# Kernel tuning notes

Hardware: AMD Instinct MI355X
Metric: run time of the kernel (lower is better)

## Reference

```python
import jax, jax.numpy as jnp
import numpy as np

LEAKY = 0.2     # PyG GATConv leaky_relu negative slope
BN_EPS = 1e-5

N, E, F_IN = 100000, 1600000, 7
ENC, HID, HEADS = 64, 32, 4
HC = HID * HEADS          # 128
DEC_IN, OUT = 64, 4
N_HIDDEN = 2              # nb_hidden_layers - 1


def gat_conv(z, src, dst, W, a_src, a_dst, b, concat):
    # PyG GATConv (shared lin for src/dst), dropout in eval mode = identity.
    n = z.shape[0]
    H, C = a_src.shape
    h = (z @ W).reshape(n, H, C)                      # [N,H,C]
    al_s = jnp.einsum('nhc,hc->nh', h, a_src)         # [N,H]
    al_d = jnp.einsum('nhc,hc->nh', h, a_dst)
    e = jax.nn.leaky_relu(al_s[src] + al_d[dst], LEAKY)   # [E,H]
    m = jax.ops.segment_max(e, dst, num_segments=n)       # scatter-softmax over in-edges
    ex = jnp.exp(e - m[dst])
    denom = jax.ops.segment_sum(ex, dst, num_segments=n)
    alpha = ex / (denom[dst] + 1e-16)                     # [E,H]
    out = jax.ops.segment_sum(h[src] * alpha[:, :, None], dst, num_segments=n)  # [N,H,C]
    out = out.reshape(n, H * C) if concat else out.mean(axis=1)
    return out + b


def batch_norm(z, gamma, beta):
    # track_running_stats=False -> always use batch statistics (biased var)
    mu = z.mean(axis=0)
    var = z.var(axis=0)
    return gamma * (z - mu) * jax.lax.rsqrt(var + BN_EPS) + beta


def setup_inputs() -> dict:
    key = jax.random.key(0)
    ks = jax.random.split(key, 20)
    g = lambda k, shape, fan: jax.random.normal(k, shape, jnp.float32) * (1.0 / np.sqrt(fan))
    inp = {
        'x': jax.random.normal(ks[0], (N, F_IN), jnp.float32),
        'edge_index': jax.random.randint(ks[1], (2, E), 0, N, jnp.int32),
        'enc_W': g(ks[2], (F_IN, ENC), F_IN),
        'enc_b': jnp.zeros((ENC,), jnp.float32),
        'in_W': g(ks[3], (ENC, HC), ENC),
        'in_att_src': g(ks[4], (HEADS, HID), HID),
        'in_att_dst': g(ks[5], (HEADS, HID), HID),
        'in_b': jnp.zeros((HC,), jnp.float32),
        'hid_W': g(ks[6], (N_HIDDEN, HC, HC), HC),
        'hid_att_src': g(ks[7], (N_HIDDEN, HEADS, HID), HID),
        'hid_att_dst': g(ks[8], (N_HIDDEN, HEADS, HID), HID),
        'hid_b': jnp.zeros((N_HIDDEN, HC), jnp.float32),
        'bn_gamma': jnp.ones((1 + N_HIDDEN, HC), jnp.float32),
        'bn_beta': jnp.zeros((1 + N_HIDDEN, HC), jnp.float32),
        'out_W': g(ks[9], (HC, DEC_IN), HC),           # out heads=1, concat=False
        'out_att_src': g(ks[10], (1, DEC_IN), DEC_IN),
        'out_att_dst': g(ks[11], (1, DEC_IN), DEC_IN),
        'out_b': jnp.zeros((DEC_IN,), jnp.float32),
        'dec_W': g(ks[12], (DEC_IN, OUT), DEC_IN),
        'dec_b': jnp.zeros((OUT,), jnp.float32),
    }
    return inp


def reference(x, edge_index, enc_W, enc_b, in_W, in_att_src, in_att_dst, in_b,
              hid_W, hid_att_src, hid_att_dst, hid_b, bn_gamma, bn_beta,
              out_W, out_att_src, out_att_dst, out_b, dec_W, dec_b):
    n = x.shape[0]
    loops = jnp.arange(n, dtype=edge_index.dtype)      # PyG GATConv add_self_loops=True
    src = jnp.concatenate([edge_index[0], loops])
    dst = jnp.concatenate([edge_index[1], loops])

    z = x @ enc_W + enc_b                              # encoder
    z = gat_conv(z, src, dst, in_W, in_att_src, in_att_dst, in_b, concat=True)
    z = jax.nn.relu(batch_norm(z, bn_gamma[0], bn_beta[0]))
    for i in range(N_HIDDEN):
        z = gat_conv(z, src, dst, hid_W[i], hid_att_src[i], hid_att_dst[i], hid_b[i], concat=True)
        z = jax.nn.relu(batch_norm(z, bn_gamma[i + 1], bn_beta[i + 1]))
    z = gat_conv(z, src, dst, out_W, out_att_src, out_att_dst, out_b, concat=False)
    z = z @ dec_W + dec_b                              # decoder
    return z
```

## Files before the change

### kernel.cpp

```cpp
#include <hip/hip_runtime.h>
#include <math.h>

#define LEAKY 0.2f
#define BN_EPS 1e-5f

typedef unsigned short u16;
typedef __bf16 bf16x8 __attribute__((ext_vector_type(8)));
typedef float f32x4 __attribute__((ext_vector_type(4)));
typedef u16 ushort8 __attribute__((ext_vector_type(8)));

__device__ __forceinline__ u16 f2bf(float x){
    unsigned u = __float_as_uint(x);
    u += 0x7FFFu + ((u >> 16) & 1u);
    return (u16)(u >> 16);
}
__device__ __forceinline__ float bf2f(u16 b){ return __uint_as_float(((unsigned)b) << 16); }


__global__ __launch_bounds__(256) void k_encoder(const float* __restrict__ x,
        const float* __restrict__ W, const float* __restrict__ b,
        float* __restrict__ z, int N){
    int gid = blockIdx.x*256 + threadIdx.x;
    int n = gid >> 6, j = gid & 63;
    if (n >= N) return;
    float acc = b[j];
    #pragma unroll
    for (int k=0;k<7;k++) acc += x[n*7+k]*W[k*64+j];
    z[(size_t)n*64+j] = acc;
}

template<int K, int M>
__global__ __launch_bounds__(256) void k_pack_w(const float* __restrict__ W,
        u16* __restrict__ hi, u16* __restrict__ lo){
    int idx = blockIdx.x*256 + threadIdx.x;
    if (idx >= K*M) return;
    int e = idx & 7, l16 = (idx >> 3) & 3, rest = idx >> 5;
    int n = rest % M, t = rest / M;
    int k = t*32 + l16*8 + e;
    float w = W[(size_t)k*M + n];
    u16 hb = f2bf(w);
    hi[idx] = hb;
    lo[idx] = f2bf(w - bf2f(hb));
}

__global__ void k_bn_coef(const float* __restrict__ cs, const float* __restrict__ cq,
        const float* __restrict__ g, const float* __restrict__ be,
        float* __restrict__ scale, float* __restrict__ shift, float invN){
    int j = threadIdx.x;
    float mu = cs[j]*invN;
    float var = cq[j]*invN - mu*mu;
    float s = g[j]*rsqrtf(var + BN_EPS);
    scale[j] = s; shift[j] = be[j] - mu*s;
}

template<int K, int M, int RW, int CW, int WR, int WC, int H, bool BNIN>
__global__ __launch_bounds__(256) void k_gemm(const float* __restrict__ z,
        const u16* __restrict__ Whi, const u16* __restrict__ Wlo,
        const float* __restrict__ bnscale, const float* __restrict__ bnshift,
        const float* __restrict__ a_src, const float* __restrict__ a_dst,
        u16* __restrict__ hout, float* __restrict__ al_s, float* __restrict__ al_d,
        int N)
{
    static_assert(RW*CW == 4 && RW*WR*16 == 64 && CW*WC*16 == M, "tile config");
    constexpr int KS = K/32;
    constexpr int KG = K/8;
    __shared__ __align__(16) u16 Ahi[64*K];
    __shared__ __align__(16) u16 Alo[64*K];
    const int brow = blockIdx.x*64;
    const int tid = threadIdx.x;

    for (int u = tid; u < 64*KG; u += 256){
        int row = u / KG, kg = u % KG;
        int gr = brow + row;
        float v[8];
        if (gr < N){
            const float4* p = (const float4*)(z + (size_t)gr*K + kg*8);
            float4 a = p[0], bq = p[1];
            v[0]=a.x; v[1]=a.y; v[2]=a.z; v[3]=a.w;
            v[4]=bq.x; v[5]=bq.y; v[6]=bq.z; v[7]=bq.w;
            if (BNIN){
                const float4* sc = (const float4*)(bnscale + kg*8);
                const float4* sh = (const float4*)(bnshift + kg*8);
                float4 s0=sc[0], s1=sc[1], t0=sh[0], t1=sh[1];
                v[0]=fmaxf(fmaf(v[0],s0.x,t0.x),0.f);
                v[1]=fmaxf(fmaf(v[1],s0.y,t0.y),0.f);
                v[2]=fmaxf(fmaf(v[2],s0.z,t0.z),0.f);
                v[3]=fmaxf(fmaf(v[3],s0.w,t0.w),0.f);
                v[4]=fmaxf(fmaf(v[4],s1.x,t1.x),0.f);
                v[5]=fmaxf(fmaf(v[5],s1.y,t1.y),0.f);
                v[6]=fmaxf(fmaf(v[6],s1.z,t1.z),0.f);
                v[7]=fmaxf(fmaf(v[7],s1.w,t1.w),0.f);
            }
        } else {
            #pragma unroll
            for (int e=0;e<8;e++) v[e]=0.f;
        }
        ushort8 h8, l8;
        #pragma unroll
        for (int e=0;e<8;e++){
            u16 hb = f2bf(v[e]);
            h8[e] = hb;
            l8[e] = f2bf(v[e] - bf2f(hb));
        }
        int rb = row >> 4, t = kg >> 2, lg = kg & 3;
        int base = (((rb*KS + t)*64) + (row & 15) + 16*lg)*8;
        *(ushort8*)&Ahi[base] = h8;
        *(ushort8*)&Alo[base] = l8;
    }
    __syncthreads();

    const int wave = tid >> 6, lane = tid & 63;
    const int wrow = wave / CW, wcol = wave % CW;
    const int l15 = lane & 15, l16 = lane >> 4;

    f32x4 acc[WR][WC];
    #pragma unroll
    for (int r=0;r<WR;r++)
        #pragma unroll
        for (int c=0;c<WC;c++) acc[r][c] = (f32x4){0.f,0.f,0.f,0.f};

    #pragma unroll
    for (int t = 0; t < KS; ++t){
        bf16x8 ah[WR], al[WR];
        #pragma unroll
        for (int r=0;r<WR;r++){
            int rb = wrow*WR + r;
            int off = ((rb*KS + t)*64 + lane)*8;
            ah[r] = *(const bf16x8*)&Ahi[off];
            al[r] = *(const bf16x8*)&Alo[off];
        }
        bf16x8 bh[WC], bl[WC];
        #pragma unroll
        for (int c=0;c<WC;c++){
            int n = (wcol*WC + c)*16 + l15;
            size_t off = ((size_t)(t*M + n)*4 + (size_t)l16)*8;
            bh[c] = *(const bf16x8*)&Whi[off];
            bl[c] = *(const bf16x8*)&Wlo[off];
        }
        #pragma unroll
        for (int r=0;r<WR;r++)
            #pragma unroll
            for (int c=0;c<WC;c++){
                acc[r][c] = __builtin_amdgcn_mfma_f32_16x16x32_bf16(al[r], bh[c], acc[r][c], 0,0,0);
                acc[r][c] = __builtin_amdgcn_mfma_f32_16x16x32_bf16(ah[r], bl[c], acc[r][c], 0,0,0);
                acc[r][c] = __builtin_amdgcn_mfma_f32_16x16x32_bf16(ah[r], bh[c], acc[r][c], 0,0,0);
            }
    }

    float as_[WC], ad_[WC];
    #pragma unroll
    for (int c=0;c<WC;c++){
        int colg = (wcol*WC + c)*16 + l15;
        as_[c] = a_src[colg]; ad_[c] = a_dst[colg];
    }
    #pragma unroll
    for (int r=0;r<WR;r++){
        #pragma unroll
        for (int q=0;q<4;q++){
            int rowg = brow + (wrow*WR + r)*16 + l16*4 + q;
            float s0=0.f,d0=0.f,s1=0.f,d1=0.f;
            #pragma unroll
            for (int c=0;c<WC;c++){
                float av = acc[r][c][q];
                if (H==1 || c < WC/2){ s0 += av*as_[c]; d0 += av*ad_[c]; }
                else                 { s1 += av*as_[c]; d1 += av*ad_[c]; }
            }
            #pragma unroll
            for (int off=1; off<16; off<<=1){
                s0 += __shfl_xor(s0, off, 64); d0 += __shfl_xor(d0, off, 64);
                if (H==4){ s1 += __shfl_xor(s1, off, 64); d1 += __shfl_xor(d1, off, 64); }
            }
            if (l15 == 0 && rowg < N){
                if (H==4){
                    al_s[(size_t)rowg*4 + wcol*2]     = s0;
                    al_s[(size_t)rowg*4 + wcol*2 + 1] = s1;
                    al_d[(size_t)rowg*4 + wcol*2]     = d0;
                    al_d[(size_t)rowg*4 + wcol*2 + 1] = d1;
                } else {
                    al_s[rowg] = s0; al_d[rowg] = d0;
                }
            }
        }
    }

    #pragma unroll
    for (int r=0;r<WR;r++)
        #pragma unroll
        for (int c=0;c<WC;c++){
            int colg = (wcol*WC + c)*16 + l15;
            #pragma unroll
            for (int q=0;q<4;q++){
                int rowg = brow + (wrow*WR + r)*16 + l16*4 + q;
                if (rowg < N) hout[(size_t)rowg*M + colg] = f2bf(acc[r][c][q]);
            }
        }
}


__global__ __launch_bounds__(256) void k_deg(const int* __restrict__ ei, int E,
        int* __restrict__ deg){
    int e = blockIdx.x*256 + threadIdx.x;
    if (e < E) atomicAdd(deg + ei[E+e], 1);
}

__device__ __forceinline__ int wave_scan(int v, int lane){
    #pragma unroll
    for (int off=1; off<64; off<<=1){
        int t = __shfl_up(v, off, 64);
        if (lane >= off) v += t;
    }
    return v;
}

__global__ __launch_bounds__(1024) void k_scan1(const int* __restrict__ deg,
        int* __restrict__ excl, int* __restrict__ bsum, int N){
    __shared__ int ws[16];
    int i = blockIdx.x*1024 + threadIdx.x;
    int lane = threadIdx.x & 63, wid = threadIdx.x >> 6;
    int v = (i < N) ? deg[i] : 0;
    int inc = wave_scan(v, lane);
    if (lane == 63) ws[wid] = inc;
    __syncthreads();
    if (wid == 0){
        int wv = (lane < 16) ? ws[lane] : 0;
        int winc = wave_scan(wv, lane);
        if (lane < 16) ws[lane] = winc - wv;
    }
    __syncthreads();
    int off = ws[wid];
    if (i < N) excl[i] = off + inc - v;
    if (threadIdx.x == 1023) bsum[blockIdx.x] = off + inc;
}

__global__ void k_scan2(int* __restrict__ bsum, int nb){
    if (threadIdx.x == 0 && blockIdx.x == 0){
        int c = 0;
        for (int i = 0; i < nb; i++){ int t = bsum[i]; bsum[i] = c; c += t; }
    }
}

__global__ __launch_bounds__(256) void k_scan3(const int* __restrict__ excl,
        const int* __restrict__ bsum, int* __restrict__ rowptr,
        int* __restrict__ cursor, int N, int E){
    int i = blockIdx.x*256 + threadIdx.x;
    if (i < N){
        int r = excl[i] + bsum[i >> 10];
        rowptr[i] = r; cursor[i] = r;
    } else if (i == N){
        rowptr[N] = E;
    }
}

__global__ __launch_bounds__(256) void k_bucket(const int* __restrict__ ei, int E,
        int* __restrict__ cursor, int* __restrict__ csr){
    int e = blockIdx.x*256 + threadIdx.x;
    if (e >= E) return;
    int pos = atomicAdd(cursor + ei[E+e], 1);
    csr[pos] = ei[e];
}


template<int H, int C, bool STATS, bool DECODE>
__global__ __launch_bounds__(256) void k_gat_agg(
        const int* __restrict__ rowptr, const int* __restrict__ csr_src,
        const float* __restrict__ al_s, const float* __restrict__ al_d,
        const u16* __restrict__ hfeat, const float* __restrict__ b,
        float* __restrict__ z, float* __restrict__ cs, float* __restrict__ cq,
        const float* __restrict__ decW, const float* __restrict__ decb,
        float* __restrict__ out, int N, int totWaves)
{
    constexpr int M = H*C;
    constexpr int EL = M/64;
    const int lane = threadIdx.x & 63;
    const int j = EL*lane;
    const int h = j / C;
    const int gw = blockIdx.x*4 + (threadIdx.x >> 6);

    const float bj0 = b[j];
    const float bj1 = (EL==2) ? b[j+1] : 0.f;
    float w0=0,w1=0,w2=0,w3=0;
    if (DECODE){ w0=decW[lane*4]; w1=decW[lane*4+1]; w2=decW[lane*4+2]; w3=decW[lane*4+3]; }
    float ls0=0.f, ls1=0.f, lq0=0.f, lq1=0.f;

    for (int dst = gw; dst < N; dst += totWaves){
        int p0 = rowptr[dst], p1 = rowptr[dst+1];
        float ald = al_d[(size_t)dst*H + h];
        float v0 = al_s[(size_t)dst*H + h] + ald;
        v0 = v0 > 0.f ? v0 : LEAKY*v0;
        float m = v0, s = 1.f;
        float acc0, acc1 = 0.f;
        if (EL==2){
            unsigned hv = *(const unsigned*)(hfeat + (size_t)dst*M + j);
            acc0 = bf2f((u16)hv); acc1 = bf2f((u16)(hv>>16));
        } else {
            acc0 = bf2f(hfeat[(size_t)dst*M + j]);
        }

        auto ld = [&](int idx, unsigned& hv, float& vs){
            if (idx < p1){
                int src = csr_src[idx];
                vs = al_s[(size_t)src*H + h];
                if (EL==2) hv = *(const unsigned*)(hfeat + (size_t)src*M + j);
                else       hv = (unsigned)hfeat[(size_t)src*M + j];
            }
        };
        auto proc = [&](unsigned hv, float vs){
            float vv = vs + ald;
            vv = vv > 0.f ? vv : LEAKY*vv;
            float mx = fmaxf(m, vv);
            float sc = __expf(m - mx);
            float ex = __expf(vv - mx);
            m = mx; s = s*sc + ex;
            acc0 = acc0*sc + bf2f((u16)hv)*ex;
            if (EL==2) acc1 = acc1*sc + bf2f((u16)(hv>>16))*ex;
        };

        unsigned hA0=0,hA1=0,hA2=0,hA3=0, hB0=0,hB1=0,hB2=0,hB3=0;
        float vA0=0,vA1=0,vA2=0,vA3=0, vB0=0,vB1=0,vB2=0,vB3=0;
        int p = p0;
        ld(p, hA0, vA0); ld(p+1, hA1, vA1); ld(p+2, hA2, vA2); ld(p+3, hA3, vA3);
        while (p < p1){
            ld(p+4, hB0, vB0); ld(p+5, hB1, vB1); ld(p+6, hB2, vB2); ld(p+7, hB3, vB3);
            proc(hA0, vA0);
            if (p+1 < p1) proc(hA1, vA1);
            if (p+2 < p1) proc(hA2, vA2);
            if (p+3 < p1) proc(hA3, vA3);
            p += 4;
            if (p >= p1) break;
            ld(p+4, hA0, vA0); ld(p+5, hA1, vA1); ld(p+6, hA2, vA2); ld(p+7, hA3, vA3);
            proc(hB0, vB0);
            if (p+1 < p1) proc(hB1, vB1);
            if (p+2 < p1) proc(hB2, vB2);
            if (p+3 < p1) proc(hB3, vB3);
            p += 4;
        }

        float inv = 1.f/(s + 1e-16f);
        float o0 = acc0*inv + bj0;
        float o1 = (EL==2) ? acc1*inv + bj1 : 0.f;
        if (STATS){ ls0+=o0; lq0+=o0*o0; ls1+=o1; lq1+=o1*o1; }
        if (!DECODE){
            if (EL==2) *(float2*)(z + (size_t)dst*M + j) = make_float2(o0,o1);
            else       z[(size_t)dst*M + j] = o0;
        } else {
            float a0=o0*w0, a1=o0*w1, a2=o0*w2, a3=o0*w3;
            #pragma unroll
            for (int off=32; off; off>>=1){
                a0 += __shfl_xor(a0, off, 64);
                a1 += __shfl_xor(a1, off, 64);
                a2 += __shfl_xor(a2, off, 64);
                a3 += __shfl_xor(a3, off, 64);
            }
            if (lane == 0){
                float4 o = make_float4(a0+decb[0], a1+decb[1], a2+decb[2], a3+decb[3]);
                *(float4*)(out + (size_t)dst*4) = o;
            }
        }
    }
    if (STATS){
        __shared__ float sls[128], slq[128];
        if (threadIdx.x < 128){ sls[threadIdx.x]=0.f; slq[threadIdx.x]=0.f; }
        __syncthreads();
        atomicAdd(&sls[j], ls0);  atomicAdd(&slq[j], lq0);
        if (EL==2){ atomicAdd(&sls[j+1], ls1); atomicAdd(&slq[j+1], lq1); }
        __syncthreads();
        if (threadIdx.x < 128){
            atomicAdd(cs + threadIdx.x, sls[threadIdx.x]);
            atomicAdd(cq + threadIdx.x, slq[threadIdx.x]);
        }
    }
}

extern "C" void kernel_launch(void* const* d_in, const int* in_sizes, int n_in,
                              void* d_out, int out_size, void* d_ws, size_t ws_size,
                              hipStream_t stream){
    const float* x      = (const float*)d_in[0];
    const int*   ei     = (const int*)  d_in[1];
    const float* enc_W  = (const float*)d_in[2];
    const float* enc_b  = (const float*)d_in[3];
    const float* in_W   = (const float*)d_in[4];
    const float* in_as  = (const float*)d_in[5];
    const float* in_ad  = (const float*)d_in[6];
    const float* in_b   = (const float*)d_in[7];
    const float* hid_W  = (const float*)d_in[8];
    const float* hid_as = (const float*)d_in[9];
    const float* hid_ad = (const float*)d_in[10];
    const float* hid_b  = (const float*)d_in[11];
    const float* bn_g   = (const float*)d_in[12];
    const float* bn_b   = (const float*)d_in[13];
    const float* out_W  = (const float*)d_in[14];
    const float* out_as = (const float*)d_in[15];
    const float* out_ad = (const float*)d_in[16];
    const float* out_b  = (const float*)d_in[17];
    const float* dec_W  = (const float*)d_in[18];
    const float* dec_b  = (const float*)d_in[19];

    const int N = in_sizes[0] / 7;
    const int E = in_sizes[1] / 2;
    const int NB = (N + 1023) / 1024;
    const int NT = (N + 63) / 64;
    const int AGG_BLOCKS = 2048, TOT_WAVES = AGG_BLOCKS*4;

    float*    bufZ   = (float*)d_ws;
    float*    al_s   = bufZ + (size_t)N*128;
    float*    al_d   = al_s + (size_t)N*4;
    float*    cs     = al_d + (size_t)N*4;
    float*    cq     = cs + 128;
    float*    scale  = cq + 128;
    float*    shift  = scale + 128;
    int*      deg    = (int*)(shift + 128);
    int*      excl   = deg + N;
    int*      rowptr = excl + N;
    int*      cursor = rowptr + (N+1);
    int*      bsum   = cursor + N;
    int*      csr    = bsum + NB;
    u16*      hb     = (u16*)(((uintptr_t)(csr + E) + 15) & ~(uintptr_t)15);
    u16*      wk     = hb + (size_t)N*128;
    u16* wk_in_hi  = wk;                    u16* wk_in_lo  = wk_in_hi  + 64*128;
    u16* wk_h0_hi  = wk_in_lo  + 64*128;    u16* wk_h0_lo  = wk_h0_hi  + 128*128;
    u16* wk_h1_hi  = wk_h0_lo  + 128*128;   u16* wk_h1_lo  = wk_h1_hi  + 128*128;
    u16* wk_out_hi = wk_h1_lo  + 128*128;   u16* wk_out_lo = wk_out_hi + 128*64;

    k_pack_w<64,128><<<(64*128+255)/256, 256, 0, stream>>>(in_W, wk_in_hi, wk_in_lo);
    k_pack_w<128,128><<<(128*128+255)/256, 256, 0, stream>>>(hid_W, wk_h0_hi, wk_h0_lo);
    k_pack_w<128,128><<<(128*128+255)/256, 256, 0, stream>>>(hid_W + 128*128, wk_h1_hi, wk_h1_lo);
    k_pack_w<128,64><<<(128*64+255)/256, 256, 0, stream>>>(out_W, wk_out_hi, wk_out_lo);

    hipMemsetAsync(deg, 0, (size_t)N*sizeof(int), stream);
    k_deg   <<<(E+255)/256, 256, 0, stream>>>(ei, E, deg);
    k_scan1 <<<NB, 1024, 0, stream>>>(deg, excl, bsum, N);
    k_scan2 <<<1, 64, 0, stream>>>(bsum, NB);
    k_scan3 <<<(N+1+255)/256, 256, 0, stream>>>(excl, bsum, rowptr, cursor, N, E);
    k_bucket<<<(E+255)/256, 256, 0, stream>>>(ei, E, cursor, csr);

    k_encoder<<<(N*64+255)/256, 256, 0, stream>>>(x, enc_W, enc_b, bufZ, N);

    const float invN = 1.f/(float)N;

    k_gemm<64,128,2,2,2,4,4,false><<<NT, 256, 0, stream>>>(bufZ, wk_in_hi, wk_in_lo,
            nullptr, nullptr, in_as, in_ad, hb, al_s, al_d, N);
    hipMemsetAsync(cs, 0, 256*sizeof(float), stream);
    k_gat_agg<4,32,true,false><<<AGG_BLOCKS, 256, 0, stream>>>(rowptr, csr, al_s, al_d,
            hb, in_b, bufZ, cs, cq, nullptr, nullptr, nullptr, N, TOT_WAVES);
    k_bn_coef<<<1, 128, 0, stream>>>(cs, cq, bn_g, bn_b, scale, shift, invN);

    for (int i = 0; i < 2; i++){
        const u16* whi = i ? wk_h1_hi : wk_h0_hi;
        const u16* wlo = i ? wk_h1_lo : wk_h0_lo;
        k_gemm<128,128,2,2,2,4,4,true><<<NT, 256, 0, stream>>>(bufZ, whi, wlo,
                scale, shift, hid_as + (size_t)i*128, hid_ad + (size_t)i*128,
                hb, al_s, al_d, N);
        hipMemsetAsync(cs, 0, 256*sizeof(float), stream);
        k_gat_agg<4,32,true,false><<<AGG_BLOCKS, 256, 0, stream>>>(rowptr, csr, al_s, al_d,
                hb, hid_b + (size_t)i*128, bufZ, cs, cq, nullptr, nullptr, nullptr, N, TOT_WAVES);
        k_bn_coef<<<1, 128, 0, stream>>>(cs, cq, bn_g + (i+1)*128, bn_b + (i+1)*128, scale, shift, invN);
    }

    k_gemm<128,64,4,1,1,4,1,true><<<NT, 256, 0, stream>>>(bufZ, wk_out_hi, wk_out_lo,
            scale, shift, out_as, out_ad, hb, al_s, al_d, N);
    k_gat_agg<1,64,false,true><<<AGG_BLOCKS, 256, 0, stream>>>(rowptr, csr, al_s, al_d,
            hb, out_b, nullptr, nullptr, nullptr, dec_W, dec_b, (float*)d_out, N, TOT_WAVES);
}
```

Measured before the change: 966.8 us.

## Replace online softmax with global per-head max bound in GAT aggregation

The GEMM kernel now computes a global per-head maximum of the source attention logits using an order-preserving uint encoding and atomicMax. The aggregation kernel uses leaky_relu(max_src + al_d[dst]) as a fixed upper bound for the softmax shift, clamped to at most 40 above the self-loop logit. This removes the running-max rescale, which costs two exps and extra multiplies per edge, and leaves one exp and FMAs per edge. The risk is underflow when an edge logit sits far below the bound. The clamp limits this but may change numerics versus the exact segment max, and one extra memset and atomic pass is added per layer.

```diff
diff --git a/kernel.cpp b/kernel.cpp
--- a/kernel.cpp
+++ b/kernel.cpp
@@ -15,6 +15,15 @@
     return (u16)(u >> 16);
 }
 __device__ __forceinline__ float bf2f(u16 b){ return __uint_as_float(((unsigned)b) << 16); }
+
+__device__ __forceinline__ unsigned enc_ord(float x){
+    unsigned u = __float_as_uint(x);
+    return (u & 0x80000000u) ? ~u : (u | 0x80000000u);
+}
+__device__ __forceinline__ float dec_ord(unsigned u){
+    unsigned b = (u & 0x80000000u) ? (u ^ 0x80000000u) : ~u;
+    return __uint_as_float(b);
+}
 
 
 __global__ __launch_bounds__(256) void k_encoder(const float* __restrict__ x,
@@ -59,7 +68,7 @@
         const float* __restrict__ bnscale, const float* __restrict__ bnshift,
         const float* __restrict__ a_src, const float* __restrict__ a_dst,
         u16* __restrict__ hout, float* __restrict__ al_s, float* __restrict__ al_d,
-        int N)
+        unsigned* __restrict__ mh, int N)
 {
     static_assert(RW*CW == 4 && RW*WR*16 == 64 && CW*WC*16 == M, "tile config");
     constexpr int KS = K/32;
@@ -153,6 +162,7 @@
         int colg = (wcol*WC + c)*16 + l15;
         as_[c] = a_src[colg]; ad_[c] = a_dst[colg];
     }
+    float wm0 = -1e30f, wm1 = -1e30f;
     #pragma unroll
     for (int r=0;r<WR;r++){
         #pragma unroll
@@ -170,6 +180,8 @@
                 s0 += __shfl_xor(s0, off, 64); d0 += __shfl_xor(d0, off, 64);
                 if (H==4){ s1 += __shfl_xor(s1, off, 64); d1 += __shfl_xor(d1, off, 64); }
             }
+            wm0 = fmaxf(wm0, s0);
+            if (H==4) wm1 = fmaxf(wm1, s1);
             if (l15 == 0 && rowg < N){
                 if (H==4){
                     al_s[(size_t)rowg*4 + wcol*2]     = s0;
@@ -181,6 +193,16 @@
                 }
             }
         }
+    }
+    wm0 = fmaxf(wm0, __shfl_xor(wm0, 16, 64));
+    wm0 = fmaxf(wm0, __shfl_xor(wm0, 32, 64));
+    if (H==4){
+        wm1 = fmaxf(wm1, __shfl_xor(wm1, 16, 64));
+        wm1 = fmaxf(wm1, __shfl_xor(wm1, 32, 64));
+    }
+    if (lane == 0){
+        atomicMax(mh + (H==4 ? wcol*2 : 0), enc_ord(wm0));
+        if (H==4) atomicMax(mh + wcol*2 + 1, enc_ord(wm1));
     }
 
     #pragma unroll
@@ -264,6 +286,7 @@
 __global__ __launch_bounds__(256) void k_gat_agg(
         const int* __restrict__ rowptr, const int* __restrict__ csr_src,
         const float* __restrict__ al_s, const float* __restrict__ al_d,
+        const unsigned* __restrict__ mh,
         const u16* __restrict__ hfeat, const float* __restrict__ b,
         float* __restrict__ z, float* __restrict__ cs, float* __restrict__ cq,
         const float* __restrict__ decW, const float* __restrict__ decb,
@@ -278,6 +301,7 @@
 
     const float bj0 = b[j];
     const float bj1 = (EL==2) ? b[j+1] : 0.f;
+    const float mhf = dec_ord(mh[h]);
     float w0=0,w1=0,w2=0,w3=0;
     if (DECODE){ w0=decW[lane*4]; w1=decW[lane*4+1]; w2=decW[lane*4+2]; w3=decW[lane*4+3]; }
     float ls0=0.f, ls1=0.f, lq0=0.f, lq1=0.f;
@@ -285,15 +309,20 @@
     for (int dst = gw; dst < N; dst += totWaves){
         int p0 = rowptr[dst], p1 = rowptr[dst+1];
         float ald = al_d[(size_t)dst*H + h];
+        float t = mhf + ald;
+        float mb = t > 0.f ? t : LEAKY*t;
         float v0 = al_s[(size_t)dst*H + h] + ald;
         v0 = v0 > 0.f ? v0 : LEAKY*v0;
-        float m = v0, s = 1.f;
+        mb = fminf(mb, v0 + 40.f);
+
+        float ex0 = __expf(v0 - mb);
+        float s = ex0;
         float acc0, acc1 = 0.f;
         if (EL==2){
             unsigned hv = *(const unsigned*)(hfeat + (size_t)dst*M + j);
-            acc0 = bf2f((u16)hv); acc1 = bf2f((u16)(hv>>16));
+            acc0 = bf2f((u16)hv)*ex0; acc1 = bf2f((u16)(hv>>16))*ex0;
         } else {
-            acc0 = bf2f(hfeat[(size_t)dst*M + j]);
+            acc0 = bf2f(hfeat[(size_t)dst*M + j])*ex0;
         }
 
         auto ld = [&](int idx, unsigned& hv, float& vs){
@@ -307,12 +336,10 @@
         auto proc = [&](unsigned hv, float vs){
             float vv = vs + ald;
             vv = vv > 0.f ? vv : LEAKY*vv;
-            float mx = fmaxf(m, vv);
-            float sc = __expf(m - mx);
-            float ex = __expf(vv - mx);
-            m = mx; s = s*sc + ex;
-            acc0 = acc0*sc + bf2f((u16)hv)*ex;
-            if (EL==2) acc1 = acc1*sc + bf2f((u16)(hv>>16))*ex;
+            float ex = __expf(vv - mb);
+            s += ex;
+            acc0 = fmaf(bf2f((u16)hv), ex, acc0);
+            if (EL==2) acc1 = fmaf(bf2f((u16)(hv>>16)), ex, acc1);
         };
 
         unsigned hA0=0,hA1=0,hA2=0,hA3=0, hB0=0,hB1=0,hB2=0,hB3=0;
@@ -335,7 +362,7 @@
             p += 4;
         }
 
-        float inv = 1.f/(s + 1e-16f);
+        float inv = 1.f/s;
         float o0 = acc0*inv + bj0;
         float o1 = (EL==2) ? acc1*inv + bj1 : 0.f;
         if (STATS){ ls0+=o0; lq0+=o0*o0; ls1+=o1; lq1+=o1*o1; }
@@ -406,7 +433,8 @@
     float*    al_d   = al_s + (size_t)N*4;
     float*    cs     = al_d + (size_t)N*4;
     float*    cq     = cs + 128;
-    float*    scale  = cq + 128;
+    unsigned* mh     = (unsigned*)(cq + 128);
+    float*    scale  = (float*)(mh + 8);
     float*    shift  = scale + 128;
     int*      deg    = (int*)(shift + 128);
     int*      excl   = deg + N;
@@ -421,6 +449,8 @@
     u16* wk_h1_hi  = wk_h0_lo  + 128*128;   u16* wk_h1_lo  = wk_h1_hi  + 128*128;
     u16* wk_out_hi = wk_h1_lo  + 128*128;   u16* wk_out_lo = wk_out_hi + 128*64;
 
+    const size_t STATS_BYTES = (128 + 128 + 8) * 4;
+
     k_pack_w<64,128><<<(64*128+255)/256, 256, 0, stream>>>(in_W, wk_in_hi, wk_in_lo);
     k_pack_w<128,128><<<(128*128+255)/256, 256, 0, stream>>>(hid_W, wk_h0_hi, wk_h0_lo);
     k_pack_w<128,128><<<(128*128+255)/256, 256, 0, stream>>>(hid_W + 128*128, wk_h1_hi, wk_h1_lo);
@@ -437,27 +467,28 @@
 
     const float invN = 1.f/(float)N;
 
+    hipMemsetAsync(cs, 0, STATS_BYTES, stream);
     k_gemm<64,128,2,2,2,4,4,false><<<NT, 256, 0, stream>>>(bufZ, wk_in_hi, wk_in_lo,
-            nullptr, nullptr, in_as, in_ad, hb, al_s, al_d, N);
-    hipMemsetAsync(cs, 0, 256*sizeof(float), stream);
-    k_gat_agg<4,32,true,false><<<AGG_BLOCKS, 256, 0, stream>>>(rowptr, csr, al_s, al_d,
+            nullptr, nullptr, in_as, in_ad, hb, al_s, al_d, mh, N);
+    k_gat_agg<4,32,true,false><<<AGG_BLOCKS, 256, 0, stream>>>(rowptr, csr, al_s, al_d, mh,
             hb, in_b, bufZ, cs, cq, nullptr, nullptr, nullptr, N, TOT_WAVES);
     k_bn_coef<<<1, 128, 0, stream>>>(cs, cq, bn_g, bn_b, scale, shift, invN);
 
     for (int i = 0; i < 2; i++){
         const u16* whi = i ? wk_h1_hi : wk_h0_hi;
         const u16* wlo = i ? wk_h1_lo : wk_h0_lo;
+        hipMemsetAsync(cs, 0, STATS_BYTES, stream);
         k_gemm<128,128,2,2,2,4,4,true><<<NT, 256, 0, stream>>>(bufZ, whi, wlo,
                 scale, shift, hid_as + (size_t)i*128, hid_ad + (size_t)i*128,
-                hb, al_s, al_d, N);
-        hipMemsetAsync(cs, 0, 256*sizeof(float), stream);
-        k_gat_agg<4,32,true,false><<<AGG_BLOCKS, 256, 0, stream>>>(rowptr, csr, al_s, al_d,
+                hb, al_s, al_d, mh, N);
+        k_gat_agg<4,32,true,false><<<AGG_BLOCKS, 256, 0, stream>>>(rowptr, csr, al_s, al_d, mh,
                 hb, hid_b + (size_t)i*128, bufZ, cs, cq, nullptr, nullptr, nullptr, N, TOT_WAVES);
         k_bn_coef<<<1, 128, 0, stream>>>(cs, cq, bn_g + (i+1)*128, bn_b + (i+1)*128, scale, shift, invN);
     }
 
+    hipMemsetAsync(cs, 0, STATS_BYTES, stream);
     k_gemm<128,64,4,1,1,4,1,true><<<NT, 256, 0, stream>>>(bufZ, wk_out_hi, wk_out_lo,
-            scale, shift, out_as, out_ad, hb, al_s, al_d, N);
-    k_gat_agg<1,64,false,true><<<AGG_BLOCKS, 256, 0, stream>>>(rowptr, csr, al_s, al_d,
+            scale, shift, out_as, out_ad, hb, al_s, al_d, mh, N);
+    k_gat_agg<1,64,false,true><<<AGG_BLOCKS, 256, 0, stream>>>(rowptr, csr, al_s, al_d, mh,
             hb, out_b, nullptr, nullptr, nullptr, dec_W, dec_b, (float*)d_out, N, TOT_WAVES);
 }
```

New measurement: 1.542 ms. 1.59x slower.

## Replace online softmax with a precomputed per-head max bound in GAT aggregation

Applied to the files above, without the earlier changes.

Adds two small reduction kernels that compute the global max of al_s per head. Each destination uses leaky_relu(max_s + al_d) as a fixed upper bound, clamped to self-loop logit + 40, so the aggregation loop drops the running-max rescale and one exp per edge. The edge loop becomes a plain exp-and-FMA accumulation. The cost is extra kernel launches and a pass over al_s, and the clamp can underflow edges whose logit sits far below the bound.

```diff
diff --git a/kernel.cpp b/kernel.cpp
--- a/kernel.cpp
+++ b/kernel.cpp
@@ -51,6 +51,41 @@
     float var = cq[j]*invN - mu*mu;
     float s = g[j]*rsqrtf(var + BN_EPS);
     scale[j] = s; shift[j] = be[j] - mu*s;
+}
+
+
+template<int H>
+__global__ __launch_bounds__(256) void k_mh1(const float* __restrict__ al,
+        float* __restrict__ pm, int total){
+    int t = threadIdx.x;
+    float m = -1e30f;
+    for (int i = blockIdx.x*256 + t; i < total; i += 64*256)
+        m = fmaxf(m, al[i]);
+    #pragma unroll
+    for (int off = H; off < 64; off <<= 1)
+        m = fmaxf(m, __shfl_xor(m, off, 64));
+    __shared__ float ws[16];
+    int lane = t & 63, wid = t >> 6;
+    if (lane < H) ws[wid*H + lane] = m;
+    __syncthreads();
+    if (t < H){
+        float mm = ws[t];
+        #pragma unroll
+        for (int w = 1; w < 4; w++) mm = fmaxf(mm, ws[w*H + t]);
+        pm[blockIdx.x*H + t] = mm;
+    }
+}
+
+template<int H>
+__global__ void k_mh2(const float* __restrict__ pm, float* __restrict__ mh){
+    int t = threadIdx.x;
+    float m = -1e30f;
+    #pragma unroll
+    for (int k = 0; k < H; k++) m = fmaxf(m, pm[t + k*64]);
+    #pragma unroll
+    for (int off = H; off < 64; off <<= 1)
+        m = fmaxf(m, __shfl_xor(m, off, 64));
+    if (t < H) mh[t] = m;
 }
 
 template<int K, int M, int RW, int CW, int WR, int WC, int H, bool BNIN>
@@ -264,6 +299,7 @@
 __global__ __launch_bounds__(256) void k_gat_agg(
         const int* __restrict__ rowptr, const int* __restrict__ csr_src,
         const float* __restrict__ al_s, const float* __restrict__ al_d,
+        const float* __restrict__ mh,
         const u16* __restrict__ hfeat, const float* __restrict__ b,
         float* __restrict__ z, float* __restrict__ cs, float* __restrict__ cq,
         const float* __restrict__ decW, const float* __restrict__ decb,
@@ -278,6 +314,7 @@
 
     const float bj0 = b[j];
     const float bj1 = (EL==2) ? b[j+1] : 0.f;
+    const float mhf = mh[h];
     float w0=0,w1=0,w2=0,w3=0;
     if (DECODE){ w0=decW[lane*4]; w1=decW[lane*4+1]; w2=decW[lane*4+2]; w3=decW[lane*4+3]; }
     float ls0=0.f, ls1=0.f, lq0=0.f, lq1=0.f;
@@ -285,15 +322,20 @@
     for (int dst = gw; dst < N; dst += totWaves){
         int p0 = rowptr[dst], p1 = rowptr[dst+1];
         float ald = al_d[(size_t)dst*H + h];
+        float t = mhf + ald;
+        float mb = t > 0.f ? t : LEAKY*t;
         float v0 = al_s[(size_t)dst*H + h] + ald;
         v0 = v0 > 0.f ? v0 : LEAKY*v0;
-        float m = v0, s = 1.f;
+        mb = fminf(mb, v0 + 40.f);
+
+        float ex0 = __expf(v0 - mb);
+        float s = ex0;
         float acc0, acc1 = 0.f;
         if (EL==2){
             unsigned hv = *(const unsigned*)(hfeat + (size_t)dst*M + j);
-            acc0 = bf2f((u16)hv); acc1 = bf2f((u16)(hv>>16));
+            acc0 = bf2f((u16)hv)*ex0; acc1 = bf2f((u16)(hv>>16))*ex0;
         } else {
-            acc0 = bf2f(hfeat[(size_t)dst*M + j]);
+            acc0 = bf2f(hfeat[(size_t)dst*M + j])*ex0;
         }
 
         auto ld = [&](int idx, unsigned& hv, float& vs){
@@ -307,12 +349,10 @@
         auto proc = [&](unsigned hv, float vs){
             float vv = vs + ald;
             vv = vv > 0.f ? vv : LEAKY*vv;
-            float mx = fmaxf(m, vv);
-            float sc = __expf(m - mx);
-            float ex = __expf(vv - mx);
-            m = mx; s = s*sc + ex;
-            acc0 = acc0*sc + bf2f((u16)hv)*ex;
-            if (EL==2) acc1 = acc1*sc + bf2f((u16)(hv>>16))*ex;
+            float ex = __expf(vv - mb);
+            s += ex;
+            acc0 = fmaf(bf2f((u16)hv), ex, acc0);
+            if (EL==2) acc1 = fmaf(bf2f((u16)(hv>>16)), ex, acc1);
         };
 
         unsigned hA0=0,hA1=0,hA2=0,hA3=0, hB0=0,hB1=0,hB2=0,hB3=0;
@@ -335,7 +375,7 @@
             p += 4;
         }
 
-        float inv = 1.f/(s + 1e-16f);
+        float inv = 1.f/s;
         float o0 = acc0*inv + bj0;
         float o1 = (EL==2) ? acc1*inv + bj1 : 0.f;
         if (STATS){ ls0+=o0; lq0+=o0*o0; ls1+=o1; lq1+=o1*o1; }
@@ -406,7 +446,9 @@
     float*    al_d   = al_s + (size_t)N*4;
     float*    cs     = al_d + (size_t)N*4;
     float*    cq     = cs + 128;
-    float*    scale  = cq + 128;
+    float*    mh     = cq + 128;
+    float*    pm     = mh + 8;
+    float*    scale  = pm + 256;
     float*    shift  = scale + 128;
     int*      deg    = (int*)(shift + 128);
     int*      excl   = deg + N;
@@ -437,27 +479,33 @@
 
     const float invN = 1.f/(float)N;
 
+    hipMemsetAsync(cs, 0, 256*sizeof(float), stream);
     k_gemm<64,128,2,2,2,4,4,false><<<NT, 256, 0, stream>>>(bufZ, wk_in_hi, wk_in_lo,
             nullptr, nullptr, in_as, in_ad, hb, al_s, al_d, N);
-    hipMemsetAsync(cs, 0, 256*sizeof(float), stream);
-    k_gat_agg<4,32,true,false><<<AGG_BLOCKS, 256, 0, stream>>>(rowptr, csr, al_s, al_d,
+    k_mh1<4><<<64, 256, 0, stream>>>(al_s, pm, N*4);
+    k_mh2<4><<<1, 64, 0, stream>>>(pm, mh);
+    k_gat_agg<4,32,true,false><<<AGG_BLOCKS, 256, 0, stream>>>(rowptr, csr, al_s, al_d, mh,
             hb, in_b, bufZ, cs, cq, nullptr, nullptr, nullptr, N, TOT_WAVES);
     k_bn_coef<<<1, 128, 0, stream>>>(cs, cq, bn_g, bn_b, scale, shift, invN);
 
     for (int i = 0; i < 2; i++){
         const u16* whi = i ? wk_h1_hi : wk_h0_hi;
         const u16* wlo = i ? wk_h1_lo : wk_h0_lo;
+        hipMemsetAsync(cs, 0, 256*sizeof(float), stream);
         k_gemm<128,128,2,2,2,4,4,true><<<NT, 256, 0, stream>>>(bufZ, whi, wlo,
                 scale, shift, hid_as + (size_t)i*128, hid_ad + (size_t)i*128,
                 hb, al_s, al_d, N);
-        hipMemsetAsync(cs, 0, 256*sizeof(float), stream);
-        k_gat_agg<4,32,true,false><<<AGG_BLOCKS, 256, 0, stream>>>(rowptr, csr, al_s, al_d,
+        k_mh1<4><<<64, 256, 0, stream>>>(al_s, pm, N*4);
+        k_mh2<4><<<1, 64, 0, stream>>>(pm, mh);
+        k_gat_agg<4,32,true,false><<<AGG_BLOCKS, 256, 0, stream>>>(rowptr, csr, al_s, al_d, mh,
                 hb, hid_b + (size_t)i*128, bufZ, cs, cq, nullptr, nullptr, nullptr, N, TOT_WAVES);
         k_bn_coef<<<1, 128, 0, stream>>>(cs, cq, bn_g + (i+1)*128, bn_b + (i+1)*128, scale, shift, invN);
     }
 
     k_gemm<128,64,4,1,1,4,1,true><<<NT, 256, 0, stream>>>(bufZ, wk_out_hi, wk_out_lo,
             scale, shift, out_as, out_ad, hb, al_s, al_d, N);
-    k_gat_agg<1,64,false,true><<<AGG_BLOCKS, 256, 0, stream>>>(rowptr, csr, al_s, al_d,
+    k_mh1<1><<<64, 256, 0, stream>>>(al_s, pm, N);
+    k_mh2<1><<<1, 64, 0, stream>>>(pm, mh);
+    k_gat_agg<1,64,false,true><<<AGG_BLOCKS, 256, 0, stream>>>(rowptr, csr, al_s, al_d, mh,
             hb, out_b, nullptr, nullptr, nullptr, dec_W, dec_b, (float*)d_out, N, TOT_WAVES);
 }
```

Measured after the change: 979.3 us. Within noise of the previous version (+1.3%).
